# Optimization experiments

Hardware: AMD Instinct MI355X
Metric: run time of the kernel (lower is better)

The kernel has to match this reference:

```python
import jax, jax.numpy as jnp
import numpy as np
import math

B, S, D, DH, R = 2, 2048, 1024, 64, 2


def _hex_grid(radius):
    coords = []
    for q in range(-radius, radius + 1):
        for r in range(max(-radius, -q - radius), min(radius, -q + radius) + 1):
            coords.append((q, r))
    return coords


def _adjacency(coords):
    idx = {c: i for i, c in enumerate(coords)}
    H = len(coords)
    A = np.zeros((H, H), dtype=np.float32)
    dirs = [(1, 0), (1, -1), (0, -1), (-1, 0), (-1, 1), (0, 1)]
    for (q, r), i in idx.items():
        for dq, dr in dirs:
            j = idx.get((q + dq, r + dr))
            if j is not None:
                A[i, j] = 1.0
    return A


def setup_inputs() -> dict:
    key = jax.random.key(0)
    ks = jax.random.split(key, 10)
    coords_list = _hex_grid(R)
    H = len(coords_list)  # 19 heads for radius 2
    coords = jnp.asarray(np.array(coords_list, dtype=np.float32))  # [H,2]
    A = _adjacency(coords_list) + np.eye(H, dtype=np.float32)      # self-loops
    adj_norm = jnp.asarray(A / A.sum(axis=1, keepdims=True))       # row-normalized [H,H]
    sd = 1.0 / math.sqrt(D)
    return {
        "x": jax.random.normal(ks[0], (B, S, D), jnp.float32),
        "coords": coords,
        "w_q": jax.random.normal(ks[1], (H, D, DH), jnp.float32) * sd,
        "w_k": jax.random.normal(ks[2], (H, D, DH), jnp.float32) * sd,
        "w_v": jax.random.normal(ks[3], (H, D, DH), jnp.float32) * sd,
        "wb1": jax.random.normal(ks[4], (2, D), jnp.float32) * 0.5,
        "bb1": jnp.zeros((D,), jnp.float32),
        "wb2": jax.random.normal(ks[5], (D, DH), jnp.float32) * sd,
        "bb2": jnp.zeros((DH,), jnp.float32),
        "w_mix": jax.random.normal(ks[6], (DH, DH), jnp.float32) / math.sqrt(DH),
        "adj_norm": adj_norm,
        "w_o": jax.random.normal(ks[7], (H * DH, D), jnp.float32) * sd,
    }


def reference(x, coords, w_q, w_k, w_v, wb1, bb1, wb2, bb2, w_mix, adj_norm, w_o):
    # coordinate bias: shared MLP mapping hex coord -> d_head bias, added to queries
    bias = jax.nn.relu(coords @ wb1 + bb1) @ wb2 + bb2          # [H,DH]
    # all heads vectorized: q/k/v [B,H,S,DH]
    q = jnp.einsum("bsd,hde->bhse", x, w_q) + bias[None, :, None, :]
    k = jnp.einsum("bsd,hde->bhse", x, w_k)
    v = jnp.einsum("bsd,hde->bhse", x, w_v)
    scores = jnp.einsum("bhse,bhte->bhst", q, k) / math.sqrt(DH)  # [B,H,S,S]
    attn = jax.nn.softmax(scores, axis=-1)
    heads = jnp.einsum("bhst,bhte->bhse", attn, v)               # [B,H,S,DH]
    # GNN mixing over the hex-grid adjacency (residual message passing)
    msg = jax.nn.relu(jnp.einsum("bhse,ef->bhsf", heads, w_mix))
    mixed = heads + jnp.einsum("hg,bgsf->bhsf", adj_norm, msg)   # [B,H,S,DH]
    # concat heads then output projection
    Bx, H, Sx, Dh = mixed.shape
    concat = jnp.transpose(mixed, (0, 2, 1, 3)).reshape(Bx, Sx, H * Dh)
    return concat @ w_o                                          # [B,S,D]
```

## Files before the change

### kernel.cpp

```cpp
#include <hip/hip_runtime.h>
#include <hip/hip_bf16.h>

#define H 19
#define Bv 2
#define Sv 2048
#define Dv 1024
#define DHv 64
#define KK2 (2*H*DHv)
#define QSCALE 0.1803368801111204f

typedef __bf16 bf16x8 __attribute__((ext_vector_type(8)));
typedef float f32x4 __attribute__((ext_vector_type(4)));

__device__ __forceinline__ ushort f2bf(float f) {
    uint u = __float_as_uint(f);
    u = (u + 0x7fffu + ((u >> 16) & 1u)) >> 16;
    return (ushort)u;
}

__device__ __forceinline__ uint cvtpk(float lo, float hi) {
    uint r;
    asm("v_cvt_pk_bf16_f32 %0, %1, %2" : "=v"(r) : "v"(lo), "v"(hi));
    return r;
}

__device__ __forceinline__ float fexp2(float x) {
#if __has_builtin(__builtin_amdgcn_exp2f)
    return __builtin_amdgcn_exp2f(x);
#else
    return exp2f(x);
#endif
}

__device__ __forceinline__ void gll16(const ushort* g, ushort* l) {
    __builtin_amdgcn_global_load_lds(
        (const __attribute__((address_space(1))) unsigned int*)g,
        (__attribute__((address_space(3))) unsigned int*)l, 16, 0, 0);
}

#define PX_N 2048
#define PW_N 912
#define PWMIX_AT (PX_N + PW_N)
#define PWO2_AT  (PWMIX_AT + 1)
#define PBIAS_AT (PWO2_AT + 304)
#define PREP_N   (PBIAS_AT + H)

__global__ __launch_bounds__(256) void prep_all(
    const float* __restrict__ x,  const float* __restrict__ wq,
    const float* __restrict__ wk, const float* __restrict__ wv,
    const float* __restrict__ wo, const float* __restrict__ adj,
    const float* __restrict__ wm, const float* __restrict__ coords,
    const float* __restrict__ wb1, const float* __restrict__ bb1,
    const float* __restrict__ wb2, const float* __restrict__ bb2,
    ushort* __restrict__ xbf, ushort* __restrict__ wpackT,
    ushort* __restrict__ wmixT, ushort* __restrict__ woTcat,
    float* __restrict__ bias)
{
    __shared__ char psm[8448];
    const int bid = blockIdx.x;
    const int tid = threadIdx.x;

    if (bid < PX_N) {
        int idx = (bid*256 + tid)*8;
        float4 a = *(const float4*)&x[idx];
        float4 b = *(const float4*)&x[idx+4];
        uint4 o;
        o.x = cvtpk(a.x, a.y); o.y = cvtpk(a.z, a.w);
        o.z = cvtpk(b.x, b.y); o.w = cvtpk(b.z, b.w);
        *(uint4*)&xbf[idx] = o;
    } else if (bid < PWMIX_AT) {
        ushort* T = (ushort*)psm;
        int i = bid - PX_N;
        int dt = i & 15, t = (i >> 4) % 3, h = (i >> 4) / 3;
        const float* w = (t == 0) ? wq : (t == 1) ? wk : wv;
        w += (size_t)h*Dv*DHv;
        int row = tid >> 2, c4 = tid & 3;
        #pragma unroll
        for (int q4 = 0; q4 < 4; ++q4) {
            float4 v = *(const float4*)&w[(size_t)(dt*64+row)*DHv + c4*16 + q4*4];
            T[(c4*16 + q4*4 + 0)*65 + row] = f2bf(v.x);
            T[(c4*16 + q4*4 + 1)*65 + row] = f2bf(v.y);
            T[(c4*16 + q4*4 + 2)*65 + row] = f2bf(v.z);
            T[(c4*16 + q4*4 + 3)*65 + row] = f2bf(v.w);
        }
        __syncthreads();
        #pragma unroll
        for (int i2 = 0; i2 < 2; ++i2) {
            int f = tid + i2*256;
            int e = f >> 3, c = f & 7;
            uint u[4];
            #pragma unroll
            for (int j = 0; j < 4; ++j) {
                uint lo = T[e*65 + c*8 + 2*j];
                uint hi = T[e*65 + c*8 + 2*j + 1];
                u[j] = lo | (hi << 16);
            }
            *(uint4*)&wpackT[((size_t)h*192 + t*64 + e)*Dv + dt*64 + c*8] = make_uint4(u[0],u[1],u[2],u[3]);
        }
    } else if (bid == PWMIX_AT) {
        int e = tid >> 2, f4 = tid & 3;
        #pragma unroll
        for (int j = 0; j < 16; ++j) {
            int f = f4*16 + j;
            wmixT[e*64 + f] = f2bf(wm[f*64 + e]);
        }
    } else if (bid < PBIAS_AT) {
        int j2 = bid - PWO2_AT;
        int nt = j2 & 15, g = j2 >> 4;
        int e = tid >> 2, n4 = tid & 3;
        float acc[16], part1[16];
        #pragma unroll
        for (int j = 0; j < 16; ++j) { acc[j] = 0.f; part1[j] = 0.f; }
        for (int h2 = 0; h2 < H; ++h2) {
            float a = adj[h2*H + g];
            const float* rp = wo + (size_t)(h2*64 + e)*Dv + nt*64 + n4*16;
            #pragma unroll
            for (int j4 = 0; j4 < 4; ++j4) {
                float4 v = *(const float4*)&rp[j4*4];
                acc[j4*4+0] += a*v.x; acc[j4*4+1] += a*v.y;
                acc[j4*4+2] += a*v.z; acc[j4*4+3] += a*v.w;
                if (h2 == g) {
                    part1[j4*4+0] = v.x; part1[j4*4+1] = v.y;
                    part1[j4*4+2] = v.z; part1[j4*4+3] = v.w;
                }
            }
        }
        #pragma unroll
        for (int j = 0; j < 16; ++j) {
            int n = nt*64 + n4*16 + j;
            woTcat[(size_t)n*KK2 + g*64 + e]         = f2bf(part1[j]);
            woTcat[(size_t)n*KK2 + H*DHv + g*64 + e] = f2bf(acc[j]);
        }
    } else {
        float* part = (float*)psm;
        int hh = bid - PBIAS_AT;
        int e = tid & 63, quar = tid >> 6;
        float c0 = coords[hh*2], c1 = coords[hh*2+1];
        float acc = (quar == 0) ? bb2[e] : 0.f;
        int d0 = quar*256;
        for (int d = d0; d < d0+256; ++d) {
            float t2 = fmaxf(c0*wb1[d] + c1*wb1[Dv+d] + bb1[d], 0.f);
            acc += t2 * wb2[d*DHv + e];
        }
        if (quar) part[(quar-1)*64 + e] = acc;
        __syncthreads();
        if (quar == 0) bias[hh*DHv + e] = acc + part[e] + part[64+e] + part[128+e];
    }
}

__global__ __launch_bounds__(256) void qkv_mfma(const ushort* __restrict__ xbf,
                                                const ushort* __restrict__ wpackT,
                                                const float* __restrict__ bias,
                                                ushort* __restrict__ qbf,
                                                ushort* __restrict__ kbf,
                                                ushort* __restrict__ vtbf) {
    const int mt = blockIdx.x, h = blockIdx.y;
    const int m0 = mt*64;
    const int tid = threadIdx.x;
    const int w = tid >> 6, lane = tid & 63;
    const int g = lane >> 4, r = lane & 15;

    __shared__ char lds[8192 + 24576];
    char* Xs = lds;
    char* Ws = lds + 8192;
    ushort* VtL = (ushort*)lds;

    f32x4 acc[4][3];
    const f32x4 zf = {0.f,0.f,0.f,0.f};
    #pragma unroll
    for (int m = 0; m < 4; ++m)
        #pragma unroll
        for (int n = 0; n < 3; ++n) acc[m][n] = zf;

    const ushort* xb = xbf + (size_t)m0*Dv;
    const ushort* wb = wpackT + (size_t)h*192*Dv;

    for (int kt = 0; kt < Dv; kt += 64) {
        __syncthreads();
        #pragma unroll
        for (int i = 0; i < 2; ++i) {
            int f = tid + i*256;
            int row = f >> 3, c = f & 7;
            *(bf16x8*)(Xs + row*128 + ((c*16) ^ ((row & 7) << 4))) =
                *(const bf16x8*)(xb + (size_t)row*Dv + kt + c*8);
        }
        #pragma unroll
        for (int i = 0; i < 6; ++i) {
            int f = tid + i*256;
            int row = f >> 3, c = f & 7;
            *(bf16x8*)(Ws + row*128 + ((c*16) ^ ((row & 7) << 4))) =
                *(const bf16x8*)(wb + (size_t)row*Dv + kt + c*8);
        }
        __syncthreads();
        #pragma unroll
        for (int kk = 0; kk < 2; ++kk) {
            bf16x8 a[4], bfr[3];
            #pragma unroll
            for (int m = 0; m < 4; ++m) {
                int row = m*16 + r;
                a[m] = *(const bf16x8*)(Xs + row*128 + (((kk*32 + g*8)*2) ^ ((row & 7) << 4)));
            }
            #pragma unroll
            for (int n = 0; n < 3; ++n) {
                int row = (w*3 + n)*16 + r;
                bfr[n] = *(const bf16x8*)(Ws + row*128 + (((kk*32 + g*8)*2) ^ ((row & 7) << 4)));
            }
            #pragma unroll
            for (int m = 0; m < 4; ++m)
                #pragma unroll
                for (int n = 0; n < 3; ++n)
                    acc[m][n] = __builtin_amdgcn_mfma_f32_16x16x32_bf16(a[m], bfr[n], acc[m][n], 0, 0, 0);
        }
    }

    __syncthreads();

    const int bb = m0 >> 11;
    const int s0 = m0 & 2047;
    #pragma unroll
    for (int m = 0; m < 4; ++m) {
        #pragma unroll
        for (int n = 0; n < 3; ++n) {
            int ng = w*3 + n;
            int t = ng >> 2;
            int e = (ng & 3)*16 + r;
            if (t == 0) {
                float bvv = bias[h*DHv + e];
                #pragma unroll
                for (int reg = 0; reg < 4; ++reg) {
                    int ss = s0 + m*16 + g*4 + reg;
                    qbf[(((size_t)bb*H + h)*Sv + ss)*DHv + e] = f2bf((acc[m][n][reg] + bvv)*QSCALE);
                }
            } else if (t == 1) {
                #pragma unroll
                for (int reg = 0; reg < 4; ++reg) {
                    int ss = s0 + m*16 + g*4 + reg;
                    kbf[(((size_t)bb*H + h)*Sv + ss)*DHv + e] = f2bf(acc[m][n][reg]);
                }
            } else {
                #pragma unroll
                for (int reg = 0; reg < 4; ++reg) {
                    int sl = m*16 + g*4 + reg;
                    VtL[e*66 + sl] = f2bf(acc[m][n][reg]);
                }
            }
        }
    }
    __syncthreads();
    #pragma unroll
    for (int i = 0; i < 2; ++i) {
        int f = tid + i*256;
        int dh = f >> 3, sc = f & 7;
        uint u[4];
        #pragma unroll
        for (int j = 0; j < 4; ++j) {
            uint lo = VtL[dh*66 + sc*8 + 2*j];
            uint hi = VtL[dh*66 + sc*8 + 2*j + 1];
            u[j] = lo | (hi << 16);
        }
        *(uint4*)&vtbf[(((size_t)bb*H + h)*DHv + dh)*Sv + s0 + sc*8] = make_uint4(u[0],u[1],u[2],u[3]);
    }
}

__global__ __launch_bounds__(256) void attn_mfma(const ushort* __restrict__ qg,
                                                 const ushort* __restrict__ kg,
                                                 const ushort* __restrict__ vtg,
                                                 const ushort* __restrict__ wmixT,
                                                 ushort* __restrict__ headsbf,
                                                 ushort* __restrict__ msgbf) {
    const int hw = blockIdx.x;
    const int logical = (hw & 7) * 152 + (hw >> 3);
    const int qt = logical & 31;
    const int hb = logical >> 5;
    const int h = hb % H, b = hb / H;

    const int tid = threadIdx.x;
    const int w = tid >> 6, lane = tid & 63;
    const int g = lane >> 4, r = lane & 15;
    const int srow = lane >> 3, scl = lane & 7;

    __shared__ ushort Ks[2][4096];
    __shared__ ushort Vs[2][4096];
    __shared__ ushort Ps[4][1024];

    const size_t bh = (size_t)b*H + h;
    const ushort* kb = kg + bh*Sv*DHv;
    const ushort* vb = vtg + bh*DHv*Sv;
    const ushort* qb = qg + (bh*Sv + qt*64 + w*16 + r)*DHv;

    bf16x8 qf0 = *(const bf16x8*)(qb + g*8);
    bf16x8 qf1 = *(const bf16x8*)(qb + 32 + g*8);

    float m_run = -1e30f, l_run = 0.f;
    f32x4 o[4];
    const f32x4 zf = {0.f,0.f,0.f,0.f};
    o[0]=zf; o[1]=zf; o[2]=zf; o[3]=zf;

    auto STAGE = [&](int jt_, int bi_) {
        #pragma unroll
        for (int is = 0; is < 2; ++is) {
            int row = w*16 + is*8 + srow;
            int kcol = (scl ^ (row & 7)) * 8;
            gll16(kb + (size_t)(jt_*64 + row)*DHv + kcol, &Ks[bi_][(w*16 + is*8)*64]);
            gll16(vb + (size_t)row*Sv + jt_*64 + kcol, &Vs[bi_][(w*16 + is*8)*64]);
        }
    };

    STAGE(0, 0);

    for (int jt = 0; jt < Sv/64; ++jt) {
        const int cur = jt & 1;
        if (jt < Sv/64 - 1) {
            STAGE(jt+1, cur^1);
            asm volatile("s_waitcnt vmcnt(4)" ::: "memory");
        } else {
            asm volatile("s_waitcnt vmcnt(0)" ::: "memory");
        }
        __builtin_amdgcn_sched_barrier(0);
        __builtin_amdgcn_s_barrier();
        __builtin_amdgcn_sched_barrier(0);

        const ushort* Kc = Ks[cur];
        const ushort* Vc = Vs[cur];

        f32x4 sc[4];
        sc[0]=zf; sc[1]=zf; sc[2]=zf; sc[3]=zf;
        #pragma unroll
        for (int kk = 0; kk < 2; ++kk) {
            bf16x8 qf = kk ? qf1 : qf0;
            #pragma unroll
            for (int nt = 0; nt < 4; ++nt) {
                int kvrow = nt*16 + r;
                bf16x8 kf = *(const bf16x8*)((const char*)Kc + kvrow*128 +
                                             ((kk*64 + g*16) ^ ((kvrow & 7) << 4)));
                sc[nt] = __builtin_amdgcn_mfma_f32_16x16x32_bf16(kf, qf, sc[nt], 0, 0, 0);
            }
        }

        float pmax = sc[0][0];
        #pragma unroll
        for (int nt = 0; nt < 4; ++nt)
            #pragma unroll
            for (int reg = 0; reg < 4; ++reg)
                pmax = fmaxf(pmax, sc[nt][reg]);
        pmax = fmaxf(pmax, __shfl_xor(pmax, 16));
        pmax = fmaxf(pmax, __shfl_xor(pmax, 32));

        if (__any(pmax > m_run + 8.0f)) {
            float mn = fmaxf(m_run, pmax);
            float corr = fexp2(m_run - mn);
            l_run *= corr;
            #pragma unroll
            for (int nt2 = 0; nt2 < 4; ++nt2) {
                o[nt2][0] *= corr; o[nt2][1] *= corr;
                o[nt2][2] *= corr; o[nt2][3] *= corr;
            }
            m_run = mn;
        }

        float lsum = 0.f;
        #pragma unroll
        for (int nt = 0; nt < 4; ++nt) {
            #pragma unroll
            for (int reg = 0; reg < 4; ++reg) {
                float p = fexp2(sc[nt][reg] - m_run);
                sc[nt][reg] = p;
                lsum += p;
            }
        }
        lsum += __shfl_xor(lsum, 16);
        lsum += __shfl_xor(lsum, 32);
        l_run += lsum;

        ushort* pw = Ps[w];
        #pragma unroll
        for (int nt = 0; nt < 4; ++nt) {
            uint u0 = cvtpk(sc[nt][0], sc[nt][1]);
            uint u1 = cvtpk(sc[nt][2], sc[nt][3]);
            int chunk = (2*nt + (g >> 1)) ^ (r & 7);
            *(uint2*)((char*)pw + r*128 + (chunk << 4) + ((g & 1)*8)) = make_uint2(u0, u1);
        }

        #pragma unroll
        for (int kk = 0; kk < 2; ++kk) {
            bf16x8 pa = *(const bf16x8*)((const char*)pw + r*128 +
                                         (((kk*4 + g) ^ (r & 7)) << 4));
            #pragma unroll
            for (int nt2 = 0; nt2 < 4; ++nt2) {
                int dh = nt2*16 + r;
                bf16x8 vf = *(const bf16x8*)((const char*)Vc + dh*128 +
                                             ((kk*64 + g*16) ^ ((dh & 7) << 4)));
                o[nt2] = __builtin_amdgcn_mfma_f32_16x16x32_bf16(vf, pa, o[nt2], 0, 0, 0);
            }
        }
        __builtin_amdgcn_sched_barrier(0);
        __builtin_amdgcn_s_barrier();
    }

    float inv = 1.0f / l_run;
    ushort* hp = headsbf + (bh*Sv + qt*64 + w*16 + r)*DHv;
    ushort* pw = Ps[w];
    #pragma unroll
    for (int nt2 = 0; nt2 < 4; ++nt2) {
        uint u0 = cvtpk(o[nt2][0]*inv, o[nt2][1]*inv);
        uint u1 = cvtpk(o[nt2][2]*inv, o[nt2][3]*inv);
        *(uint2*)(hp + nt2*16 + g*4) = make_uint2(u0, u1);
        int chunk = (2*nt2 + (g >> 1)) ^ (r & 7);
        *(uint2*)((char*)pw + r*128 + (chunk << 4) + ((g & 1)*8)) = make_uint2(u0, u1);
    }

    bf16x8 wmf[2][4];
    #pragma unroll
    for (int kk = 0; kk < 2; ++kk)
        #pragma unroll
        for (int nt = 0; nt < 4; ++nt)
            wmf[kk][nt] = *(const bf16x8*)(wmixT + (nt*16 + r)*64 + kk*32 + g*8);

    f32x4 macc[4];
    macc[0]=zf; macc[1]=zf; macc[2]=zf; macc[3]=zf;
    #pragma unroll
    for (int kk = 0; kk < 2; ++kk) {
        bf16x8 pa = *(const bf16x8*)((const char*)pw + r*128 +
                                     (((kk*4 + g) ^ (r & 7)) << 4));
        #pragma unroll
        for (int nt = 0; nt < 4; ++nt)
            macc[nt] = __builtin_amdgcn_mfma_f32_16x16x32_bf16(wmf[kk][nt], pa, macc[nt], 0, 0, 0);
    }
    ushort* mp = msgbf + (bh*Sv + qt*64 + w*16 + r)*DHv;
    #pragma unroll
    for (int nt = 0; nt < 4; ++nt) {
        uint u0 = cvtpk(fmaxf(macc[nt][0], 0.f), fmaxf(macc[nt][1], 0.f));
        uint u1 = cvtpk(fmaxf(macc[nt][2], 0.f), fmaxf(macc[nt][3], 0.f));
        *(uint2*)(mp + nt*16 + g*4) = make_uint2(u0, u1);
    }
}

__global__ __launch_bounds__(256) void out_mfma(const ushort* __restrict__ headsbf,
                                                const ushort* __restrict__ msgbf,
                                                const ushort* __restrict__ woTcat,
                                                float* __restrict__ out) {
    const int mt = blockIdx.x, nt2 = blockIdx.y;
    const int m0 = mt*64, n0 = nt2*128;
    const int tid = threadIdx.x;
    const int w = tid >> 6, lane = tid & 63;
    const int g = lane >> 4, r = lane & 15;

    __shared__ char lds[8192 + 16384];
    char* As = lds;
    char* Bs = lds + 8192;

    const int b = m0 >> 11;
    const int s0 = m0 & 2047;

    f32x4 acc[8];
    const f32x4 zf = {0.f,0.f,0.f,0.f};
    #pragma unroll
    for (int n = 0; n < 8; ++n) acc[n] = zf;

    for (int ktile = 0; ktile < KK2/64; ++ktile) {
        const int hh = (ktile < H) ? ktile : ktile - H;
        const ushort* asrc = ((ktile < H) ? headsbf : msgbf) +
                             ((size_t)((size_t)b*H + hh)*Sv + s0)*DHv;
        __syncthreads();
        #pragma unroll
        for (int i = 0; i < 2; ++i) {
            int f = tid + i*256;
            int row = f >> 3, c = f & 7;
            *(bf16x8*)(As + row*128 + ((c*16) ^ ((row & 7) << 4))) =
                *(const bf16x8*)(asrc + (size_t)row*DHv + c*8);
        }
        #pragma unroll
        for (int i = 0; i < 4; ++i) {
            int f = tid + i*256;
            int row = f >> 3, c = f & 7;
            *(bf16x8*)(Bs + row*128 + ((c*16) ^ ((row & 7) << 4))) =
                *(const bf16x8*)(woTcat + (size_t)(n0 + row)*KK2 + ktile*64 + c*8);
        }
        __syncthreads();
        #pragma unroll
        for (int kk = 0; kk < 2; ++kk) {
            int arow = w*16 + r;
            bf16x8 a = *(const bf16x8*)(As + arow*128 + (((kk*32 + g*8)*2) ^ ((arow & 7) << 4)));
            #pragma unroll
            for (int n = 0; n < 8; ++n) {
                int brow = n*16 + r;
                bf16x8 bfr = *(const bf16x8*)(Bs + brow*128 + (((kk*32 + g*8)*2) ^ ((brow & 7) << 4)));
                acc[n] = __builtin_amdgcn_mfma_f32_16x16x32_bf16(a, bfr, acc[n], 0, 0, 0);
            }
        }
    }

    #pragma unroll
    for (int n = 0; n < 8; ++n) {
        #pragma unroll
        for (int reg = 0; reg < 4; ++reg) {
            int grow = m0 + w*16 + g*4 + reg;
            out[(size_t)grow*Dv + n0 + n*16 + r] = acc[n][reg];
        }
    }
}

extern "C" void kernel_launch(void* const* d_in, const int* in_sizes, int n_in,
                              void* d_out, int out_size, void* d_ws, size_t ws_size,
                              hipStream_t stream) {
    const float* x      = (const float*)d_in[0];
    const float* coords = (const float*)d_in[1];
    const float* w_q    = (const float*)d_in[2];
    const float* w_k    = (const float*)d_in[3];
    const float* w_v    = (const float*)d_in[4];
    const float* wb1    = (const float*)d_in[5];
    const float* bb1    = (const float*)d_in[6];
    const float* wb2    = (const float*)d_in[7];
    const float* bb2    = (const float*)d_in[8];
    const float* w_mix  = (const float*)d_in[9];
    const float* adj    = (const float*)d_in[10];
    const float* w_o    = (const float*)d_in[11];

    char* ws = (char*)d_ws;
    const size_t QKV_BYTES = (size_t)Bv*H*Sv*DHv*2;
    const size_t XBF_BYTES = (size_t)Bv*Sv*Dv*2;
    const size_t WPK_BYTES = (size_t)H*192*Dv*2;

    size_t off = 0;
    float*  bias  = (float*)(ws + off);  off += 16384;
    ushort* qbf   = (ushort*)(ws + off); off += QKV_BYTES;
    ushort* kbf   = (ushort*)(ws + off); off += QKV_BYTES;
    ushort* vtbf  = (ushort*)(ws + off); off += QKV_BYTES;
    ushort* hdbf  = (ushort*)(ws + off); off += QKV_BYTES;
    ushort* xbf   = (ushort*)(ws + off);
    ushort* msgbf = xbf;
    off += XBF_BYTES;
    ushort* wpkT  = (ushort*)(ws + off); off += WPK_BYTES;
    ushort* wmixT = (ushort*)(ws + off); off += 8192;
    ushort* woTc  = (ushort*)(ws + off); off += (size_t)Dv*KK2*2;
    float*  out   = (float*)d_out;

    prep_all<<<PREP_N, 256, 0, stream>>>(x, w_q, w_k, w_v, w_o, adj, w_mix,
                                         coords, wb1, bb1, wb2, bb2,
                                         xbf, wpkT, wmixT, woTc, bias);
    qkv_mfma<<<dim3(64, H), 256, 0, stream>>>(xbf, wpkT, bias, qbf, kbf, vtbf);
    attn_mfma<<<1216, 256, 0, stream>>>(qbf, kbf, vtbf, wmixT, hdbf, msgbf);
    out_mfma<<<dim3(64, 8), 256, 0, stream>>>(hdbf, msgbf, woTc, out);
}
```

Before: 356.9 us.

## Single-buffer attention K/V tiles and coalesce prep woTcat writes via LDS

The attention loop stops prefetching the next K/V tile into a second LDS buffer. It now loads each tile synchronously into a single buffer between two barriers. This halves K/V LDS usage, possibly raising occupancy, but exposes global load latency every iteration. The prep kernel reorders its block roles so the heavy bias and w_o blocks start first. It also stages the transposed w_o output in LDS so the stores are coalesced 16-byte writes.

```diff
diff --git a/kernel.cpp b/kernel.cpp
--- a/kernel.cpp
+++ b/kernel.cpp
@@ -38,12 +38,12 @@
         (__attribute__((address_space(3))) unsigned int*)l, 16, 0, 0);
 }
 
-#define PX_N 2048
-#define PW_N 912
-#define PWMIX_AT (PX_N + PW_N)
-#define PWO2_AT  (PWMIX_AT + 1)
-#define PBIAS_AT (PWO2_AT + 304)
-#define PREP_N   (PBIAS_AT + H)
+#define PBIAS_AT 0
+#define PWO2_AT  (PBIAS_AT + H)
+#define PWMIX_AT (PWO2_AT + 304)
+#define PWPK_AT  (PWMIX_AT + 1)
+#define PX_AT    (PWPK_AT + 912)
+#define PREP_N   (PX_AT + 2048)
 
 __global__ __launch_bounds__(256) void prep_all(
     const float* __restrict__ x,  const float* __restrict__ wq,
@@ -56,82 +56,11 @@
     ushort* __restrict__ wmixT, ushort* __restrict__ woTcat,
     float* __restrict__ bias)
 {
-    __shared__ char psm[8448];
+    __shared__ char psm[18432];
     const int bid = blockIdx.x;
     const int tid = threadIdx.x;
 
-    if (bid < PX_N) {
-        int idx = (bid*256 + tid)*8;
-        float4 a = *(const float4*)&x[idx];
-        float4 b = *(const float4*)&x[idx+4];
-        uint4 o;
-        o.x = cvtpk(a.x, a.y); o.y = cvtpk(a.z, a.w);
-        o.z = cvtpk(b.x, b.y); o.w = cvtpk(b.z, b.w);
-        *(uint4*)&xbf[idx] = o;
-    } else if (bid < PWMIX_AT) {
-        ushort* T = (ushort*)psm;
-        int i = bid - PX_N;
-        int dt = i & 15, t = (i >> 4) % 3, h = (i >> 4) / 3;
-        const float* w = (t == 0) ? wq : (t == 1) ? wk : wv;
-        w += (size_t)h*Dv*DHv;
-        int row = tid >> 2, c4 = tid & 3;
-        #pragma unroll
-        for (int q4 = 0; q4 < 4; ++q4) {
-            float4 v = *(const float4*)&w[(size_t)(dt*64+row)*DHv + c4*16 + q4*4];
-            T[(c4*16 + q4*4 + 0)*65 + row] = f2bf(v.x);
-            T[(c4*16 + q4*4 + 1)*65 + row] = f2bf(v.y);
-            T[(c4*16 + q4*4 + 2)*65 + row] = f2bf(v.z);
-            T[(c4*16 + q4*4 + 3)*65 + row] = f2bf(v.w);
-        }
-        __syncthreads();
-        #pragma unroll
-        for (int i2 = 0; i2 < 2; ++i2) {
-            int f = tid + i2*256;
-            int e = f >> 3, c = f & 7;
-            uint u[4];
-            #pragma unroll
-            for (int j = 0; j < 4; ++j) {
-                uint lo = T[e*65 + c*8 + 2*j];
-                uint hi = T[e*65 + c*8 + 2*j + 1];
-                u[j] = lo | (hi << 16);
-            }
-            *(uint4*)&wpackT[((size_t)h*192 + t*64 + e)*Dv + dt*64 + c*8] = make_uint4(u[0],u[1],u[2],u[3]);
-        }
-    } else if (bid == PWMIX_AT) {
-        int e = tid >> 2, f4 = tid & 3;
-        #pragma unroll
-        for (int j = 0; j < 16; ++j) {
-            int f = f4*16 + j;
-            wmixT[e*64 + f] = f2bf(wm[f*64 + e]);
-        }
-    } else if (bid < PBIAS_AT) {
-        int j2 = bid - PWO2_AT;
-        int nt = j2 & 15, g = j2 >> 4;
-        int e = tid >> 2, n4 = tid & 3;
-        float acc[16], part1[16];
-        #pragma unroll
-        for (int j = 0; j < 16; ++j) { acc[j] = 0.f; part1[j] = 0.f; }
-        for (int h2 = 0; h2 < H; ++h2) {
-            float a = adj[h2*H + g];
-            const float* rp = wo + (size_t)(h2*64 + e)*Dv + nt*64 + n4*16;
-            #pragma unroll
-            for (int j4 = 0; j4 < 4; ++j4) {
-                float4 v = *(const float4*)&rp[j4*4];
-                acc[j4*4+0] += a*v.x; acc[j4*4+1] += a*v.y;
-                acc[j4*4+2] += a*v.z; acc[j4*4+3] += a*v.w;
-                if (h2 == g) {
-                    part1[j4*4+0] = v.x; part1[j4*4+1] = v.y;
-                    part1[j4*4+2] = v.z; part1[j4*4+3] = v.w;
-                }
-            }
-        }
-        #pragma unroll
-        for (int j = 0; j < 16; ++j) {
-            int n = nt*64 + n4*16 + j;
-            woTcat[(size_t)n*KK2 + g*64 + e]         = f2bf(part1[j]);
-            woTcat[(size_t)n*KK2 + H*DHv + g*64 + e] = f2bf(acc[j]);
-        }
-    } else {
+    if (bid < PWO2_AT) {
         float* part = (float*)psm;
         int hh = bid - PBIAS_AT;
         int e = tid & 63, quar = tid >> 6;
@@ -145,6 +74,92 @@
         if (quar) part[(quar-1)*64 + e] = acc;
         __syncthreads();
         if (quar == 0) bias[hh*DHv + e] = acc + part[e] + part[64+e] + part[128+e];
+    } else if (bid < PWMIX_AT) {
+        int j2 = bid - PWO2_AT;
+        int nt = j2 & 15, g = j2 >> 4;
+        int e = tid >> 2, n4 = tid & 3;
+        float acc[16], part1[16];
+        #pragma unroll
+        for (int j = 0; j < 16; ++j) { acc[j] = 0.f; part1[j] = 0.f; }
+        for (int h2 = 0; h2 < H; ++h2) {
+            float a = adj[h2*H + g];
+            const float* rp = wo + (size_t)(h2*64 + e)*Dv + nt*64 + n4*16;
+            #pragma unroll
+            for (int j4 = 0; j4 < 4; ++j4) {
+                float4 v = *(const float4*)&rp[j4*4];
+                acc[j4*4+0] += a*v.x; acc[j4*4+1] += a*v.y;
+                acc[j4*4+2] += a*v.z; acc[j4*4+3] += a*v.w;
+                if (h2 == g) {
+                    part1[j4*4+0] = v.x; part1[j4*4+1] = v.y;
+                    part1[j4*4+2] = v.z; part1[j4*4+3] = v.w;
+                }
+            }
+        }
+        ushort* T = (ushort*)psm;
+        #pragma unroll
+        for (int j = 0; j < 16; ++j) {
+            int nl = n4*16 + j;
+            T[nl*72 + e]         = f2bf(part1[j]);
+            T[64*72 + nl*72 + e] = f2bf(acc[j]);
+        }
+        __syncthreads();
+        int nl = tid >> 2, c = tid & 3;
+        {
+            ushort* dst = &woTcat[(size_t)(nt*64 + nl)*KK2 + g*64 + c*16];
+            uint4 v0 = *(uint4*)&T[nl*72 + c*16];
+            uint4 v1 = *(uint4*)&T[nl*72 + c*16 + 8];
+            *(uint4*)dst = v0; *(uint4*)(dst + 8) = v1;
+        }
+        {
+            ushort* dst = &woTcat[(size_t)(nt*64 + nl)*KK2 + H*DHv + g*64 + c*16];
+            uint4 v0 = *(uint4*)&T[64*72 + nl*72 + c*16];
+            uint4 v1 = *(uint4*)&T[64*72 + nl*72 + c*16 + 8];
+            *(uint4*)dst = v0; *(uint4*)(dst + 8) = v1;
+        }
+    } else if (bid == PWMIX_AT) {
+        int e = tid >> 2, f4 = tid & 3;
+        #pragma unroll
+        for (int j = 0; j < 16; ++j) {
+            int f = f4*16 + j;
+            wmixT[e*64 + f] = f2bf(wm[f*64 + e]);
+        }
+    } else if (bid < PX_AT) {
+        ushort* T = (ushort*)psm;
+        int i = bid - PWPK_AT;
+        int dt = i & 15, t = (i >> 4) % 3, h = (i >> 4) / 3;
+        const float* w = (t == 0) ? wq : (t == 1) ? wk : wv;
+        w += (size_t)h*Dv*DHv;
+        int row = tid >> 2, c4 = tid & 3;
+        #pragma unroll
+        for (int q4 = 0; q4 < 4; ++q4) {
+            float4 v = *(const float4*)&w[(size_t)(dt*64+row)*DHv + c4*16 + q4*4];
+            T[(c4*16 + q4*4 + 0)*65 + row] = f2bf(v.x);
+            T[(c4*16 + q4*4 + 1)*65 + row] = f2bf(v.y);
+            T[(c4*16 + q4*4 + 2)*65 + row] = f2bf(v.z);
+            T[(c4*16 + q4*4 + 3)*65 + row] = f2bf(v.w);
+        }
+        __syncthreads();
+        #pragma unroll
+        for (int i2 = 0; i2 < 2; ++i2) {
+            int f = tid + i2*256;
+            int e = f >> 3, c = f & 7;
+            uint u[4];
+            #pragma unroll
+            for (int j = 0; j < 4; ++j) {
+                uint lo = T[e*65 + c*8 + 2*j];
+                uint hi = T[e*65 + c*8 + 2*j + 1];
+                u[j] = lo | (hi << 16);
+            }
+            *(uint4*)&wpackT[((size_t)h*192 + t*64 + e)*Dv + dt*64 + c*8] = make_uint4(u[0],u[1],u[2],u[3]);
+        }
+    } else {
+        int idx = ((bid - PX_AT)*256 + tid)*8;
+        float4 a = *(const float4*)&x[idx];
+        float4 b = *(const float4*)&x[idx+4];
+        uint4 o;
+        o.x = cvtpk(a.x, a.y); o.y = cvtpk(a.z, a.w);
+        o.z = cvtpk(b.x, b.y); o.w = cvtpk(b.z, b.w);
+        *(uint4*)&xbf[idx] = o;
     }
 }
 
@@ -279,8 +294,8 @@
     const int g = lane >> 4, r = lane & 15;
     const int srow = lane >> 3, scl = lane & 7;
 
-    __shared__ ushort Ks[2][4096];
-    __shared__ ushort Vs[2][4096];
+    __shared__ ushort Ks[4096];
+    __shared__ ushort Vs[4096];
     __shared__ ushort Ps[4][1024];
 
     const size_t bh = (size_t)b*H + h;
@@ -296,32 +311,17 @@
     const f32x4 zf = {0.f,0.f,0.f,0.f};
     o[0]=zf; o[1]=zf; o[2]=zf; o[3]=zf;
 
-    auto STAGE = [&](int jt_, int bi_) {
+    for (int jt = 0; jt < Sv/64; ++jt) {
+        __syncthreads();
         #pragma unroll
         for (int is = 0; is < 2; ++is) {
             int row = w*16 + is*8 + srow;
             int kcol = (scl ^ (row & 7)) * 8;
-            gll16(kb + (size_t)(jt_*64 + row)*DHv + kcol, &Ks[bi_][(w*16 + is*8)*64]);
-            gll16(vb + (size_t)row*Sv + jt_*64 + kcol, &Vs[bi_][(w*16 + is*8)*64]);
-        }
-    };
-
-    STAGE(0, 0);
-
-    for (int jt = 0; jt < Sv/64; ++jt) {
-        const int cur = jt & 1;
-        if (jt < Sv/64 - 1) {
-            STAGE(jt+1, cur^1);
-            asm volatile("s_waitcnt vmcnt(4)" ::: "memory");
-        } else {
-            asm volatile("s_waitcnt vmcnt(0)" ::: "memory");
-        }
-        __builtin_amdgcn_sched_barrier(0);
-        __builtin_amdgcn_s_barrier();
-        __builtin_amdgcn_sched_barrier(0);
-
-        const ushort* Kc = Ks[cur];
-        const ushort* Vc = Vs[cur];
+            gll16(kb + (size_t)(jt*64 + row)*DHv + kcol, &Ks[(w*16 + is*8)*64]);
+            gll16(vb + (size_t)row*Sv + jt*64 + kcol, &Vs[(w*16 + is*8)*64]);
+        }
+        asm volatile("s_waitcnt vmcnt(0)" ::: "memory");
+        __syncthreads();
 
         f32x4 sc[4];
         sc[0]=zf; sc[1]=zf; sc[2]=zf; sc[3]=zf;
@@ -331,7 +331,7 @@
             #pragma unroll
             for (int nt = 0; nt < 4; ++nt) {
                 int kvrow = nt*16 + r;
-                bf16x8 kf = *(const bf16x8*)((const char*)Kc + kvrow*128 +
+                bf16x8 kf = *(const bf16x8*)((const char*)Ks + kvrow*128 +
                                              ((kk*64 + g*16) ^ ((kvrow & 7) << 4)));
                 sc[nt] = __builtin_amdgcn_mfma_f32_16x16x32_bf16(kf, qf, sc[nt], 0, 0, 0);
             }
@@ -388,13 +388,11 @@
             #pragma unroll
             for (int nt2 = 0; nt2 < 4; ++nt2) {
                 int dh = nt2*16 + r;
-                bf16x8 vf = *(const bf16x8*)((const char*)Vc + dh*128 +
+                bf16x8 vf = *(const bf16x8*)((const char*)Vs + dh*128 +
                                              ((kk*64 + g*16) ^ ((dh & 7) << 4)));
                 o[nt2] = __builtin_amdgcn_mfma_f32_16x16x32_bf16(vf, pa, o[nt2], 0, 0, 0);
             }
         }
-        __builtin_amdgcn_sched_barrier(0);
-        __builtin_amdgcn_s_barrier();
     }
 
     float inv = 1.0f / l_run;
```

Result: faster. 345.4 us (-3.2%).
